# Performance work log

Measured on AMD Instinct MI355X. Metric: run time of the kernel, lower is better.

Reference implementation:

```python
import jax, jax.numpy as jnp
import numpy as np

K = 3        # kernel_size
UM = 2       # um_dim
EPS = 1e-6
SLOPE = 0.01 # F.leaky_relu default negative slope


def setup_inputs() -> dict:
    key = jax.random.key(0)
    k1, k2, k3 = jax.random.split(key, 3)
    B, C, H, Wd = 16, 64, 64, 64
    O = 64
    xx = jax.random.normal(k1, (B, C, H, Wd), dtype=jnp.float32)
    W = jax.random.normal(k2, (O, C, K, K), dtype=jnp.float32) * 0.05
    b = jax.random.normal(k3, (O,), dtype=jnp.float32) * 0.05
    return {"xx": xx, "W": W, "b": b}


def reference(xx, W, b):
    B, C, H, Wd = xx.shape
    O = W.shape[0]
    p = (K - 1) // 2
    # replicate pad (mode='replicate' in torch == 'edge' in numpy/jax)
    xp = jnp.pad(xx, ((0, 0), (0, 0), (p, p), (p, p)), mode='edge')
    # unfold -> patches[b, c, i, j, h, w] = xp[b, c, h+i, w+j]; stride==1
    pats = jnp.stack(
        [xp[:, :, i:i + H, j:j + Wd] for i in range(K) for j in range(K)],
        axis=2,
    ).reshape(B, C, K, K, H, Wd)
    # min-max "std" normalization over (channel-group, ki, kj)
    g = pats.reshape(B, C // UM, UM, K, K, H, Wd)
    stds = (g.max(axis=(1, 3, 4), keepdims=True)
            - g.min(axis=(1, 3, 4), keepdims=True))  # [B,1,UM,1,1,H,W]
    normed = (g / (stds + EPS)).reshape(B, C, K, K, H, Wd)
    # patch-conv with stride=k on the unfolded image is equivalent to this
    # per-position contraction; big[b,c,h*k+j, w*k+i] = normed[b,c,i,j,h,w]
    # so the kernel indexes as W[o, c, j, i].
    out = jnp.einsum('bcijhw,ocji->bohw', normed, W) + b[None, :, None, None]
    out = jnp.where(out >= 0, out, SLOPE * out)  # leaky_relu
    # inverse transform: re-scale by (stds + eps)
    stds_s = stds.reshape(B, 1, UM, H, Wd)
    out = out.reshape(B, O // UM, UM, H, Wd) * (stds_s + EPS)
    return out.reshape(B, O, H, Wd)
```

## Files before the change

kernel.cpp:

```cpp
#include <hip/hip_runtime.h>
#include <hip/hip_bf16.h>

#define B_  16
#define C_  64
#define H_  64
#define W_  64
#define O_  64
#define EPS 1e-6f
#define SLOPE 0.01f

typedef __bf16  bf16x8 __attribute__((ext_vector_type(8)));
typedef float   f32x4  __attribute__((ext_vector_type(4)));

#define XT_OFF   0
#define XT_SZ    36864
#define PMIN_OFF 36864
#define PMAX_OFF 38912
#define SINV_OFF 40960
#define SEPS_OFF 43008
#define SMEM_SZ  45056

__device__ __forceinline__ unsigned short f2bf(float f) {
  unsigned u = __float_as_uint(f);
  u += 0x7fffu + ((u >> 16) & 1u);
  return (unsigned short)(u >> 16);
}

__device__ __forceinline__ int clampi(int v, int lo, int hi) {
  return v < lo ? lo : (v > hi ? hi : v);
}

__global__ void wtransform_kernel(const float* __restrict__ Wsrc,
                                  unsigned short* __restrict__ Wt) {
  int idx = blockIdx.x * 256 + threadIdx.x;
  if (idx >= O_ * C_ * 9) return;
  int i = idx % 3;
  int j = (idx / 3) % 3;
  int c = (idx / 9) % C_;
  int o = idx / (9 * C_);
  int tap = i * 3 + j;
  Wt[((tap * 2 + (c & 1)) * 64 + o) * 32 + (c >> 1)] = f2bf(Wsrc[idx]);
}

__launch_bounds__(256, 3)
__global__ void conv_main_kernel(const float* __restrict__ x,
                                 const unsigned short* __restrict__ Wt,
                                 const float* __restrict__ bias,
                                 float* __restrict__ out) {
  __shared__ char smem[SMEM_SZ];
  const int tid  = threadIdx.x;
  const int lane = tid & 63;
  const int wv   = tid >> 6;
  const int b    = blockIdx.x >> 5;
  const int h0   = (blockIdx.x & 31) << 1;

  {
    const int w = tid & 63;
    const int r = tid >> 6;
    const int hr = clampi(h0 - 1 + r, 0, H_ - 1);
    const float* xb = x + ((size_t)b * C_ * H_ * W_) + hr * W_ + w;
    float mn[2] = {3.4e38f, 3.4e38f}, mx[2] = {-3.4e38f, -3.4e38f};
    #pragma unroll
    for (int pm = 0; pm < 8; ++pm) {
      const int p = pm >> 2, m = pm & 3;
      unsigned d[4];
      #pragma unroll
      for (int e = 0; e < 4; ++e) {
        const int c2a = m * 8 + 2 * e;
        const float f0 = xb[(2 * c2a + p) * (H_ * W_)];
        const float f1 = xb[(2 * (c2a + 1) + p) * (H_ * W_)];
        mn[p] = fminf(mn[p], fminf(f0, f1));
        mx[p] = fmaxf(mx[p], fmaxf(f0, f1));
        d[e] = (unsigned)f2bf(f0) | ((unsigned)f2bf(f1) << 16);
      }
      *(uint4*)(smem + XT_OFF + (r * 64 + w) * 144 + p * 64 + m * 16) =
          make_uint4(d[0], d[1], d[2], d[3]);
    }
    ((float*)(smem + PMIN_OFF))[(0 * 4 + r) * 64 + w] = mn[0];
    ((float*)(smem + PMIN_OFF))[(1 * 4 + r) * 64 + w] = mn[1];
    ((float*)(smem + PMAX_OFF))[(0 * 4 + r) * 64 + w] = mx[0];
    ((float*)(smem + PMAX_OFF))[(1 * 4 + r) * 64 + w] = mx[1];
  }
  __syncthreads();

  {
    const int hh = tid >> 7, p = (tid >> 6) & 1, w = tid & 63;
    const float* pmin = (const float*)(smem + PMIN_OFF);
    const float* pmax = (const float*)(smem + PMAX_OFF);
    float mn = 3.4e38f, mx = -3.4e38f;
    #pragma unroll
    for (int r = 0; r < 3; ++r) {
      #pragma unroll
      for (int dw = -1; dw <= 1; ++dw) {
        const int wc = clampi(w + dw, 0, W_ - 1);
        mn = fminf(mn, pmin[(p * 4 + (hh + r)) * 64 + wc]);
        mx = fmaxf(mx, pmax[(p * 4 + (hh + r)) * 64 + wc]);
      }
    }
    const float sv = (mx - mn) + EPS;
    ((float*)(smem + SEPS_OFF))[(hh * 2 + p) * 64 + w] = sv;
    ((float*)(smem + SINV_OFF))[(hh * 2 + p) * 64 + w] = 1.0f / sv;
  }
  __syncthreads();

  const int o0  = wv * 16;
  const int l15 = lane & 15;
  const int q   = lane >> 4;
  const float* sinv = (const float*)(smem + SINV_OFF);

  const f32x4 zero = {0.0f, 0.0f, 0.0f, 0.0f};
  f32x4 oacc[2][4];
  #pragma unroll
  for (int hh = 0; hh < 2; ++hh)
    #pragma unroll
    for (int nt = 0; nt < 4; ++nt) oacc[hh][nt] = zero;

  #pragma unroll 1
  for (int p = 0; p < 2; ++p) {
    bf16x8 af[9];
    #pragma unroll
    for (int t9 = 0; t9 < 9; ++t9)
      af[t9] = *(const bf16x8*)(Wt + ((t9 * 2 + p) * 64 + o0 + l15) * 32 + q * 8);

    f32x4 acc[2][4];
    #pragma unroll
    for (int hh = 0; hh < 2; ++hh)
      #pragma unroll
      for (int nt = 0; nt < 4; ++nt) acc[hh][nt] = zero;

    #pragma unroll
    for (int xr = 0; xr < 4; ++xr) {
      #pragma unroll
      for (int nt = 0; nt < 4; ++nt) {
        bf16x8 bfr[3];
        #pragma unroll
        for (int j = 0; j < 3; ++j) {
          const int wc = clampi(nt * 16 + l15 + j - 1, 0, W_ - 1);
          bfr[j] = *(const bf16x8*)(smem + XT_OFF + (xr * 64 + wc) * 144 + p * 64 + q * 16);
        }
        #pragma unroll
        for (int hh = 0; hh < 2; ++hh) {
          const int i = xr - hh;
          if (i >= 0 && i < 3) {
            #pragma unroll
            for (int j = 0; j < 3; ++j)
              acc[hh][nt] = __builtin_amdgcn_mfma_f32_16x16x32_bf16(
                  af[i * 3 + j], bfr[j], acc[hh][nt], 0, 0, 0);
          }
        }
      }
    }

    #pragma unroll
    for (int hh = 0; hh < 2; ++hh) {
      #pragma unroll
      for (int nt = 0; nt < 4; ++nt) {
        const float sv = sinv[(hh * 2 + p) * 64 + nt * 16 + l15];
        #pragma unroll
        for (int reg = 0; reg < 4; ++reg)
          oacc[hh][nt][reg] += acc[hh][nt][reg] * sv;
      }
    }
  }

  const float* seps = (const float*)(smem + SEPS_OFF);
  float bv[4];
  #pragma unroll
  for (int reg = 0; reg < 4; ++reg) bv[reg] = bias[o0 + q * 4 + reg];

  #pragma unroll
  for (int hh = 0; hh < 2; ++hh) {
    #pragma unroll
    for (int nt = 0; nt < 4; ++nt) {
      const int wpx = nt * 16 + l15;
      const float se0 = seps[(hh * 2 + 0) * 64 + wpx];
      const float se1 = seps[(hh * 2 + 1) * 64 + wpx];
      #pragma unroll
      for (int reg = 0; reg < 4; ++reg) {
        const int o = o0 + q * 4 + reg;
        float v = oacc[hh][nt][reg] + bv[reg];
        v = v >= 0.0f ? v : SLOPE * v;
        v *= (reg & 1) ? se1 : se0;
        out[((b * O_ + o) * H_ + (h0 + hh)) * W_ + wpx] = v;
      }
    }
  }
}

extern "C" void kernel_launch(void* const* d_in, const int* in_sizes, int n_in,
                              void* d_out, int out_size, void* d_ws, size_t ws_size,
                              hipStream_t stream) {
  const float* x    = (const float*)d_in[0];
  const float* Wsrc = (const float*)d_in[1];
  const float* bias = (const float*)d_in[2];
  float* out = (float*)d_out;
  unsigned short* Wt = (unsigned short*)d_ws;

  wtransform_kernel<<<144, 256, 0, stream>>>(Wsrc, Wt);
  conv_main_kernel<<<512, 256, 0, stream>>>(x, Wt, bias, out);
}
```

Measured before the change: 83.50 us.

## Stage input rows via global_load_lds and preload all weight fragments upfront

The input staging now issues async global-to-LDS loads (global_load_lds) into a raw fp32 buffer, two rows per pass, then converts to bf16 and computes partial min/max from LDS using a split over channel halves. All 18 weight fragments are loaded into registers at kernel start so their latency overlaps the staging, and the p loop is fully unrolled. LDS use grows to about 78 KB and the launch bound drops from 3 to 2 blocks per CU, trading occupancy for fewer strided global loads.

```diff
diff --git a/kernel.cpp b/kernel.cpp
--- a/kernel.cpp
+++ b/kernel.cpp
@@ -14,11 +14,13 @@
 
 #define XT_OFF   0
 #define XT_SZ    36864
-#define PMIN_OFF 36864
-#define PMAX_OFF 38912
-#define SINV_OFF 40960
-#define SEPS_OFF 43008
-#define SMEM_SZ  45056
+#define RAW_OFF  36864
+#define RAW_SZ   32768
+#define PMIN_OFF 69632
+#define PMAX_OFF 73728
+#define SINV_OFF 77824
+#define SEPS_OFF 78848
+#define SMEM_SZ  79872
 
 __device__ __forceinline__ unsigned short f2bf(float f) {
   unsigned u = __float_as_uint(f);
@@ -42,7 +44,7 @@
   Wt[((tap * 2 + (c & 1)) * 64 + o) * 32 + (c >> 1)] = f2bf(Wsrc[idx]);
 }
 
-__launch_bounds__(256, 3)
+__launch_bounds__(256, 2)
 __global__ void conv_main_kernel(const float* __restrict__ x,
                                  const unsigned short* __restrict__ Wt,
                                  const float* __restrict__ bias,
@@ -53,38 +55,71 @@
   const int wv   = tid >> 6;
   const int b    = blockIdx.x >> 5;
   const int h0   = (blockIdx.x & 31) << 1;
+  const int l15  = lane & 15;
+  const int q    = lane >> 4;
+  const int o0   = wv * 16;
+
+  bf16x8 af[2][9];
+  #pragma unroll
+  for (int p = 0; p < 2; ++p)
+    #pragma unroll
+    for (int t9 = 0; t9 < 9; ++t9)
+      af[p][t9] = *(const bf16x8*)(Wt + ((t9 * 2 + p) * 64 + o0 + l15) * 32 + q * 8);
+
+  const int w  = tid & 63;
+  const int rc = tid >> 6;
+  const int rloc_t = rc & 1;
+  const int cs = rc >> 1;
+
+  #pragma unroll 1
+  for (int rp = 0; rp < 2; ++rp) {
+    #pragma unroll
+    for (int it = 0; it < 32; ++it) {
+      const int idx  = wv * 32 + it;
+      const int rl   = idx >> 6;
+      const int c    = idx & 63;
+      const int hr   = clampi(h0 - 1 + rp * 2 + rl, 0, H_ - 1);
+      const float* g = x + (((b * C_ + c) * H_ + hr) * W_) + lane;
+      __builtin_amdgcn_global_load_lds(
+          (const __attribute__((address_space(1))) unsigned*)g,
+          (__attribute__((address_space(3))) unsigned*)(smem + RAW_OFF + (rl * 64 + c) * 256),
+          4, 0, 0);
+    }
+    asm volatile("s_waitcnt vmcnt(0)" ::: "memory");
+    __syncthreads();
+
+    {
+      const int r = rp * 2 + rloc_t;
+      const float* rawp = (const float*)(smem + RAW_OFF) + rloc_t * 4096 + w;
+      float mn[2] = {3.4e38f, 3.4e38f}, mx[2] = {-3.4e38f, -3.4e38f};
+      unsigned pk[2][8];
+      #pragma unroll
+      for (int k = 0; k < 32; ++k) {
+        const int c = cs * 32 + k;
+        const float f = rawp[c * 64];
+        const int p = k & 1;
+        const int u = k >> 1;
+        mn[p] = fminf(mn[p], f);
+        mx[p] = fmaxf(mx[p], f);
+        const unsigned h = f2bf(f);
+        if (u & 1) pk[p][u >> 1] |= (h << 16);
+        else       pk[p][u >> 1]  = h;
+      }
+      char* xtw = smem + XT_OFF + (r * 64 + w) * 144 + cs * 32;
+      *(uint4*)(xtw)      = make_uint4(pk[0][0], pk[0][1], pk[0][2], pk[0][3]);
+      *(uint4*)(xtw + 16) = make_uint4(pk[0][4], pk[0][5], pk[0][6], pk[0][7]);
+      *(uint4*)(xtw + 64) = make_uint4(pk[1][0], pk[1][1], pk[1][2], pk[1][3]);
+      *(uint4*)(xtw + 80) = make_uint4(pk[1][4], pk[1][5], pk[1][6], pk[1][7]);
+      ((float*)(smem + PMIN_OFF))[((0 * 4 + r) * 2 + cs) * 64 + w] = mn[0];
+      ((float*)(smem + PMIN_OFF))[((1 * 4 + r) * 2 + cs) * 64 + w] = mn[1];
+      ((float*)(smem + PMAX_OFF))[((0 * 4 + r) * 2 + cs) * 64 + w] = mx[0];
+      ((float*)(smem + PMAX_OFF))[((1 * 4 + r) * 2 + cs) * 64 + w] = mx[1];
+    }
+    __syncthreads();
+  }
 
   {
-    const int w = tid & 63;
-    const int r = tid >> 6;
-    const int hr = clampi(h0 - 1 + r, 0, H_ - 1);
-    const float* xb = x + ((size_t)b * C_ * H_ * W_) + hr * W_ + w;
-    float mn[2] = {3.4e38f, 3.4e38f}, mx[2] = {-3.4e38f, -3.4e38f};
-    #pragma unroll
-    for (int pm = 0; pm < 8; ++pm) {
-      const int p = pm >> 2, m = pm & 3;
-      unsigned d[4];
-      #pragma unroll
-      for (int e = 0; e < 4; ++e) {
-        const int c2a = m * 8 + 2 * e;
-        const float f0 = xb[(2 * c2a + p) * (H_ * W_)];
-        const float f1 = xb[(2 * (c2a + 1) + p) * (H_ * W_)];
-        mn[p] = fminf(mn[p], fminf(f0, f1));
-        mx[p] = fmaxf(mx[p], fmaxf(f0, f1));
-        d[e] = (unsigned)f2bf(f0) | ((unsigned)f2bf(f1) << 16);
-      }
-      *(uint4*)(smem + XT_OFF + (r * 64 + w) * 144 + p * 64 + m * 16) =
-          make_uint4(d[0], d[1], d[2], d[3]);
-    }
-    ((float*)(smem + PMIN_OFF))[(0 * 4 + r) * 64 + w] = mn[0];
-    ((float*)(smem + PMIN_OFF))[(1 * 4 + r) * 64 + w] = mn[1];
-    ((float*)(smem + PMAX_OFF))[(0 * 4 + r) * 64 + w] = mx[0];
-    ((float*)(smem + PMAX_OFF))[(1 * 4 + r) * 64 + w] = mx[1];
-  }
-  __syncthreads();
-
-  {
-    const int hh = tid >> 7, p = (tid >> 6) & 1, w = tid & 63;
+    const int hh = tid >> 7, p = (tid >> 6) & 1, ww = tid & 63;
     const float* pmin = (const float*)(smem + PMIN_OFF);
     const float* pmax = (const float*)(smem + PMAX_OFF);
     float mn = 3.4e38f, mx = -3.4e38f;
@@ -92,22 +127,21 @@
     for (int r = 0; r < 3; ++r) {
       #pragma unroll
       for (int dw = -1; dw <= 1; ++dw) {
-        const int wc = clampi(w + dw, 0, W_ - 1);
-        mn = fminf(mn, pmin[(p * 4 + (hh + r)) * 64 + wc]);
-        mx = fmaxf(mx, pmax[(p * 4 + (hh + r)) * 64 + wc]);
+        const int wc = clampi(ww + dw, 0, W_ - 1);
+        #pragma unroll
+        for (int c2s = 0; c2s < 2; ++c2s) {
+          mn = fminf(mn, pmin[((p * 4 + (hh + r)) * 2 + c2s) * 64 + wc]);
+          mx = fmaxf(mx, pmax[((p * 4 + (hh + r)) * 2 + c2s) * 64 + wc]);
+        }
       }
     }
     const float sv = (mx - mn) + EPS;
-    ((float*)(smem + SEPS_OFF))[(hh * 2 + p) * 64 + w] = sv;
-    ((float*)(smem + SINV_OFF))[(hh * 2 + p) * 64 + w] = 1.0f / sv;
+    ((float*)(smem + SEPS_OFF))[(hh * 2 + p) * 64 + ww] = sv;
+    ((float*)(smem + SINV_OFF))[(hh * 2 + p) * 64 + ww] = 1.0f / sv;
   }
   __syncthreads();
 
-  const int o0  = wv * 16;
-  const int l15 = lane & 15;
-  const int q   = lane >> 4;
   const float* sinv = (const float*)(smem + SINV_OFF);
-
   const f32x4 zero = {0.0f, 0.0f, 0.0f, 0.0f};
   f32x4 oacc[2][4];
   #pragma unroll
@@ -115,13 +149,8 @@
     #pragma unroll
     for (int nt = 0; nt < 4; ++nt) oacc[hh][nt] = zero;
 
-  #pragma unroll 1
+  #pragma unroll
   for (int p = 0; p < 2; ++p) {
-    bf16x8 af[9];
-    #pragma unroll
-    for (int t9 = 0; t9 < 9; ++t9)
-      af[t9] = *(const bf16x8*)(Wt + ((t9 * 2 + p) * 64 + o0 + l15) * 32 + q * 8);
-
     f32x4 acc[2][4];
     #pragma unroll
     for (int hh = 0; hh < 2; ++hh)
@@ -145,14 +174,14 @@
             #pragma unroll
             for (int j = 0; j < 3; ++j)
               acc[hh][nt] = __builtin_amdgcn_mfma_f32_16x16x32_bf16(
-                  af[i * 3 + j], bfr[j], acc[hh][nt], 0, 0, 0);
+                  af[p][i * 3 + j], bfr[j], acc[hh][nt], 0, 0, 0);
           }
         }
       }
     }
 
     #pragma unroll
-    for (int hh = 0; hh < 2; ++hh) {
+    for (int hh = 0; hh < 2; ++hh)
       #pragma unroll
       for (int nt = 0; nt < 4; ++nt) {
         const float sv = sinv[(hh * 2 + p) * 64 + nt * 16 + l15];
@@ -160,7 +189,6 @@
         for (int reg = 0; reg < 4; ++reg)
           oacc[hh][nt][reg] += acc[hh][nt][reg] * sv;
       }
-    }
   }
 
   const float* seps = (const float*)(smem + SEPS_OFF);
```

New measurement: 83.46 us. About the same (-0.1%).

## Fuse weight bf16 transform into conv kernel and use one output row per block

Applied to the files above, without the earlier changes.

Removes the separate weight-transform kernel launch. Each block now reads fp32 weights directly from global memory with strided scalar loads and converts them to bf16 in registers. Blocks now compute a single output row instead of two, which doubles the grid to 1024 blocks and reduces shared memory use. The trade-off is that input-row loading is more redundant (3 halo rows per output row instead of 4 per 2), and every block repeats the uncoalesced weight loads and conversion.

```diff
diff --git a/kernel.cpp b/kernel.cpp
--- a/kernel.cpp
+++ b/kernel.cpp
@@ -13,12 +13,12 @@
 typedef float   f32x4  __attribute__((ext_vector_type(4)));
 
 #define XT_OFF   0
-#define XT_SZ    36864
-#define PMIN_OFF 36864
-#define PMAX_OFF 38912
-#define SINV_OFF 40960
-#define SEPS_OFF 43008
-#define SMEM_SZ  45056
+#define XT_SZ    27648
+#define PMIN_OFF 27648
+#define PMAX_OFF 29184
+#define SINV_OFF 30720
+#define SEPS_OFF 31232
+#define SMEM_SZ  31744
 
 __device__ __forceinline__ unsigned short f2bf(float f) {
   unsigned u = __float_as_uint(f);
@@ -30,34 +30,25 @@
   return v < lo ? lo : (v > hi ? hi : v);
 }
 
-__global__ void wtransform_kernel(const float* __restrict__ Wsrc,
-                                  unsigned short* __restrict__ Wt) {
-  int idx = blockIdx.x * 256 + threadIdx.x;
-  if (idx >= O_ * C_ * 9) return;
-  int i = idx % 3;
-  int j = (idx / 3) % 3;
-  int c = (idx / 9) % C_;
-  int o = idx / (9 * C_);
-  int tap = i * 3 + j;
-  Wt[((tap * 2 + (c & 1)) * 64 + o) * 32 + (c >> 1)] = f2bf(Wsrc[idx]);
-}
-
 __launch_bounds__(256, 3)
-__global__ void conv_main_kernel(const float* __restrict__ x,
-                                 const unsigned short* __restrict__ Wt,
-                                 const float* __restrict__ bias,
-                                 float* __restrict__ out) {
+__global__ void conv_fused_kernel(const float* __restrict__ x,
+                                  const float* __restrict__ Wsrc,
+                                  const float* __restrict__ bias,
+                                  float* __restrict__ out) {
   __shared__ char smem[SMEM_SZ];
   const int tid  = threadIdx.x;
   const int lane = tid & 63;
   const int wv   = tid >> 6;
-  const int b    = blockIdx.x >> 5;
-  const int h0   = (blockIdx.x & 31) << 1;
+  const int b    = blockIdx.x >> 6;
+  const int h    = blockIdx.x & 63;
+  const int l15  = lane & 15;
+  const int q    = lane >> 4;
+  const int o0   = wv * 16;
 
-  {
+  if (wv < 3) {
     const int w = tid & 63;
-    const int r = tid >> 6;
-    const int hr = clampi(h0 - 1 + r, 0, H_ - 1);
+    const int r = wv;
+    const int hr = clampi(h - 1 + r, 0, H_ - 1);
     const float* xb = x + ((size_t)b * C_ * H_ * W_) + hr * W_ + w;
     float mn[2] = {3.4e38f, 3.4e38f}, mx[2] = {-3.4e38f, -3.4e38f};
     #pragma unroll
@@ -76,15 +67,15 @@
       *(uint4*)(smem + XT_OFF + (r * 64 + w) * 144 + p * 64 + m * 16) =
           make_uint4(d[0], d[1], d[2], d[3]);
     }
-    ((float*)(smem + PMIN_OFF))[(0 * 4 + r) * 64 + w] = mn[0];
-    ((float*)(smem + PMIN_OFF))[(1 * 4 + r) * 64 + w] = mn[1];
-    ((float*)(smem + PMAX_OFF))[(0 * 4 + r) * 64 + w] = mx[0];
-    ((float*)(smem + PMAX_OFF))[(1 * 4 + r) * 64 + w] = mx[1];
+    ((float*)(smem + PMIN_OFF))[(0 * 3 + r) * 64 + w] = mn[0];
+    ((float*)(smem + PMIN_OFF))[(1 * 3 + r) * 64 + w] = mn[1];
+    ((float*)(smem + PMAX_OFF))[(0 * 3 + r) * 64 + w] = mx[0];
+    ((float*)(smem + PMAX_OFF))[(1 * 3 + r) * 64 + w] = mx[1];
   }
   __syncthreads();
 
-  {
-    const int hh = tid >> 7, p = (tid >> 6) & 1, w = tid & 63;
+  if (tid < 128) {
+    const int p = tid >> 6, ww = tid & 63;
     const float* pmin = (const float*)(smem + PMIN_OFF);
     const float* pmax = (const float*)(smem + PMAX_OFF);
     float mn = 3.4e38f, mx = -3.4e38f;
@@ -92,74 +83,69 @@
     for (int r = 0; r < 3; ++r) {
       #pragma unroll
       for (int dw = -1; dw <= 1; ++dw) {
-        const int wc = clampi(w + dw, 0, W_ - 1);
-        mn = fminf(mn, pmin[(p * 4 + (hh + r)) * 64 + wc]);
-        mx = fmaxf(mx, pmax[(p * 4 + (hh + r)) * 64 + wc]);
+        const int wc = clampi(ww + dw, 0, W_ - 1);
+        mn = fminf(mn, pmin[(p * 3 + r) * 64 + wc]);
+        mx = fmaxf(mx, pmax[(p * 3 + r) * 64 + wc]);
       }
     }
     const float sv = (mx - mn) + EPS;
-    ((float*)(smem + SEPS_OFF))[(hh * 2 + p) * 64 + w] = sv;
-    ((float*)(smem + SINV_OFF))[(hh * 2 + p) * 64 + w] = 1.0f / sv;
+    ((float*)(smem + SEPS_OFF))[p * 64 + ww] = sv;
+    ((float*)(smem + SINV_OFF))[p * 64 + ww] = 1.0f / sv;
   }
   __syncthreads();
 
-  const int o0  = wv * 16;
-  const int l15 = lane & 15;
-  const int q   = lane >> 4;
   const float* sinv = (const float*)(smem + SINV_OFF);
+  const f32x4 zero = {0.0f, 0.0f, 0.0f, 0.0f};
+  f32x4 oacc[4];
+  #pragma unroll
+  for (int nt = 0; nt < 4; ++nt) oacc[nt] = zero;
 
-  const f32x4 zero = {0.0f, 0.0f, 0.0f, 0.0f};
-  f32x4 oacc[2][4];
-  #pragma unroll
-  for (int hh = 0; hh < 2; ++hh)
-    #pragma unroll
-    for (int nt = 0; nt < 4; ++nt) oacc[hh][nt] = zero;
+  const float* wbase = Wsrc + (o0 + l15) * 576;
 
   #pragma unroll 1
   for (int p = 0; p < 2; ++p) {
-    bf16x8 af[9];
+    f32x4 acc[4];
     #pragma unroll
-    for (int t9 = 0; t9 < 9; ++t9)
-      af[t9] = *(const bf16x8*)(Wt + ((t9 * 2 + p) * 64 + o0 + l15) * 32 + q * 8);
-
-    f32x4 acc[2][4];
-    #pragma unroll
-    for (int hh = 0; hh < 2; ++hh)
-      #pragma unroll
-      for (int nt = 0; nt < 4; ++nt) acc[hh][nt] = zero;
+    for (int nt = 0; nt < 4; ++nt) acc[nt] = zero;
 
     #pragma unroll
-    for (int xr = 0; xr < 4; ++xr) {
+    for (int i = 0; i < 3; ++i) {
+      bf16x8 af3[3];
+      #pragma unroll
+      for (int j = 0; j < 3; ++j) {
+        union { uint4 u; bf16x8 v; } cvt;
+        unsigned pk[4];
+        #pragma unroll
+        for (int eo = 0; eo < 4; ++eo) {
+          const float f0 = wbase[(2 * (q * 8 + 2 * eo) + p) * 9 + j * 3 + i];
+          const float f1 = wbase[(2 * (q * 8 + 2 * eo + 1) + p) * 9 + j * 3 + i];
+          pk[eo] = (unsigned)f2bf(f0) | ((unsigned)f2bf(f1) << 16);
+        }
+        cvt.u = make_uint4(pk[0], pk[1], pk[2], pk[3]);
+        af3[j] = cvt.v;
+      }
+      const char* row = smem + XT_OFF + (i * 64) * 144 + p * 64 + q * 16;
       #pragma unroll
       for (int nt = 0; nt < 4; ++nt) {
         bf16x8 bfr[3];
         #pragma unroll
         for (int j = 0; j < 3; ++j) {
           const int wc = clampi(nt * 16 + l15 + j - 1, 0, W_ - 1);
-          bfr[j] = *(const bf16x8*)(smem + XT_OFF + (xr * 64 + wc) * 144 + p * 64 + q * 16);
+          bfr[j] = *(const bf16x8*)(row + wc * 144);
         }
         #pragma unroll
-        for (int hh = 0; hh < 2; ++hh) {
-          const int i = xr - hh;
-          if (i >= 0 && i < 3) {
-            #pragma unroll
-            for (int j = 0; j < 3; ++j)
-              acc[hh][nt] = __builtin_amdgcn_mfma_f32_16x16x32_bf16(
-                  af[i * 3 + j], bfr[j], acc[hh][nt], 0, 0, 0);
-          }
-        }
+        for (int j = 0; j < 3; ++j)
+          acc[nt] = __builtin_amdgcn_mfma_f32_16x16x32_bf16(
+              af3[j], bfr[j], acc[nt], 0, 0, 0);
       }
     }
 
     #pragma unroll
-    for (int hh = 0; hh < 2; ++hh) {
+    for (int nt = 0; nt < 4; ++nt) {
+      const float sv = sinv[p * 64 + nt * 16 + l15];
       #pragma unroll
-      for (int nt = 0; nt < 4; ++nt) {
-        const float sv = sinv[(hh * 2 + p) * 64 + nt * 16 + l15];
-        #pragma unroll
-        for (int reg = 0; reg < 4; ++reg)
-          oacc[hh][nt][reg] += acc[hh][nt][reg] * sv;
-      }
+      for (int reg = 0; reg < 4; ++reg)
+        oacc[nt][reg] += acc[nt][reg] * sv;
     }
   }
 
@@ -169,20 +155,17 @@
   for (int reg = 0; reg < 4; ++reg) bv[reg] = bias[o0 + q * 4 + reg];
 
   #pragma unroll
-  for (int hh = 0; hh < 2; ++hh) {
+  for (int nt = 0; nt < 4; ++nt) {
+    const int wpx = nt * 16 + l15;
+    const float se0 = seps[0 * 64 + wpx];
+    const float se1 = seps[1 * 64 + wpx];
     #pragma unroll
-    for (int nt = 0; nt < 4; ++nt) {
-      const int wpx = nt * 16 + l15;
-      const float se0 = seps[(hh * 2 + 0) * 64 + wpx];
-      const float se1 = seps[(hh * 2 + 1) * 64 + wpx];
-      #pragma unroll
-      for (int reg = 0; reg < 4; ++reg) {
-        const int o = o0 + q * 4 + reg;
-        float v = oacc[hh][nt][reg] + bv[reg];
-        v = v >= 0.0f ? v : SLOPE * v;
-        v *= (reg & 1) ? se1 : se0;
-        out[((b * O_ + o) * H_ + (h0 + hh)) * W_ + wpx] = v;
-      }
+    for (int reg = 0; reg < 4; ++reg) {
+      const int o = o0 + q * 4 + reg;
+      float v = oacc[nt][reg] + bv[reg];
+      v = v >= 0.0f ? v : SLOPE * v;
+      v *= (reg & 1) ? se1 : se0;
+      out[(((size_t)b * O_ + o) * H_ + h) * W_ + wpx] = v;
     }
   }
 }
@@ -194,8 +177,7 @@
   const float* Wsrc = (const float*)d_in[1];
   const float* bias = (const float*)d_in[2];
   float* out = (float*)d_out;
-  unsigned short* Wt = (unsigned short*)d_ws;
+  (void)d_ws; (void)ws_size;
 
-  wtransform_kernel<<<144, 256, 0, stream>>>(Wsrc, Wt);
-  conv_main_kernel<<<512, 256, 0, stream>>>(x, Wt, bias, out);
+  conv_fused_kernel<<<1024, 256, 0, stream>>>(x, Wsrc, bias, out);
 }
```

After: 107.9 us. 29.2% more time.
